# Kernel optimization log

Hardware: AMD Instinct MI355X
Metric: run time of the kernel (lower is better)

Reference implementation:

```python
import jax, jax.numpy as jnp
import numpy as np

N = 50000       # nodes
E = 1600000     # edges
G = 16          # graphs in batch
NUMCHIP = 16    # node features
NUMEDGE = 8     # edge features
H = 32          # hidden_channels
NEG = 0.2       # LeakyReLU slope (PyG GAT default)


def _wegat_conv(x, ea, src, dst, Wn, bn, We, be, att):
    """Edge-weighted GAT conv: returns (node_out [N,H], edge_out [E,NUMEDGE])."""
    xn = x @ Wn + bn                      # [N, H]
    ea2 = ea @ We + be                    # [E, NUMEDGE]
    xi = xn[dst]                          # [E, H] target features
    xj = xn[src]                          # [E, H] source features
    logits = jnp.concatenate([xi, xj, ea2], axis=-1) @ att   # [E]
    logits = jax.nn.leaky_relu(logits, NEG)
    # numerically stable softmax over incoming edges per destination node
    m = jax.ops.segment_max(logits, dst, num_segments=N)
    m = jnp.where(jnp.isfinite(m), m, 0.0)
    p = jnp.exp(logits - m[dst])
    s = jax.ops.segment_sum(p, dst, num_segments=N)
    alpha = p / (s[dst] + 1e-16)          # [E]
    out = jax.ops.segment_sum(xj * alpha[:, None], dst, num_segments=N)  # [N, H]
    return out, ea2


def setup_inputs() -> dict:
    key = jax.random.key(0)
    ks = jax.random.split(key, 24)

    def gl(k, shape):
        fan_in = shape[0] if len(shape) > 1 else shape[0]
        return jax.random.normal(k, shape, dtype=jnp.float32) * (1.0 / np.sqrt(fan_in))

    inp = {
        'x': jax.random.normal(ks[0], (N, NUMCHIP), dtype=jnp.float32),
        'edge_attr': jax.random.normal(ks[1], (E, NUMEDGE), dtype=jnp.float32),
        'edge_index': jax.random.randint(ks[2], (2, E), 0, N, dtype=jnp.int64),
        'batch': jnp.sort(jax.random.randint(ks[3], (N,), 0, G, dtype=jnp.int64)),
        # layer 1
        'Wn1': gl(ks[4], (NUMCHIP, H)), 'bn1': jnp.zeros((H,), jnp.float32),
        'We1': gl(ks[5], (NUMEDGE, NUMEDGE)), 'be1': jnp.zeros((NUMEDGE,), jnp.float32),
        'att1': gl(ks[6], (2 * H + NUMEDGE,)),
        # layer 2
        'Wn2': gl(ks[7], (H, H)), 'bn2': jnp.zeros((H,), jnp.float32),
        'We2': gl(ks[8], (NUMEDGE, NUMEDGE)), 'be2': jnp.zeros((NUMEDGE,), jnp.float32),
        'att2': gl(ks[9], (2 * H + NUMEDGE,)),
        # layer 3
        'Wn3': gl(ks[10], (H, H)), 'bn3': jnp.zeros((H,), jnp.float32),
        'We3': gl(ks[11], (NUMEDGE, NUMEDGE)), 'be3': jnp.zeros((NUMEDGE,), jnp.float32),
        'att3': gl(ks[12], (2 * H + NUMEDGE,)),
        # head
        'Wlin': gl(ks[13], (H, 1)), 'blin': jnp.zeros((1,), jnp.float32),
    }
    return inp


def reference(x, edge_attr, edge_index, batch,
              Wn1, bn1, We1, be1, att1,
              Wn2, bn2, We2, be2, att2,
              Wn3, bn3, We3, be3, att3,
              Wlin, blin):
    src, dst = edge_index[0], edge_index[1]
    x1, ea1 = _wegat_conv(x, edge_attr, src, dst, Wn1, bn1, We1, be1, att1)
    x1 = jax.nn.relu(x1)  # NOTE: original's edge_attr.relu() is a discarded no-op
    x2, ea2 = _wegat_conv(x1, ea1, src, dst, Wn2, bn2, We2, be2, att2)
    x2 = jax.nn.relu(x2)
    x3, _ = _wegat_conv(x2, ea2, src, dst, Wn3, bn3, We3, be3, att3)
    # global mean pool over graphs
    sums = jax.ops.segment_sum(x3, batch, num_segments=G)                   # [G, H]
    cnts = jax.ops.segment_sum(jnp.ones((N,), x3.dtype), batch, num_segments=G)
    pooled = sums / jnp.maximum(cnts, 1.0)[:, None]
    return pooled @ Wlin + blin  # [G, 1]
```

## Files before the change

kernel.cpp:

```cpp
#include <hip/hip_runtime.h>
#include <math.h>


__global__ __launch_bounds__(256) void hist_kernel(const int* __restrict__ dst, int* cnt, int E) {
    int e = blockIdx.x * blockDim.x + threadIdx.x;
    if (e < E) atomicAdd(&cnt[dst[e]], 1);
}

__global__ __launch_bounds__(1024) void scan_kernel(const int* __restrict__ cnt,
                                                    int* rowptr, int* cursor, int n) {
    __shared__ int sums[1024];
    int t = threadIdx.x;
    int CH = (n + 1023) >> 10;
    int s0 = t * CH;
    int s1 = min(n, s0 + CH);
    int local = 0;
    for (int i = s0; i < s1; i++) local += cnt[i];
    sums[t] = local;
    __syncthreads();
    for (int off = 1; off < 1024; off <<= 1) {
        int v = (t >= off) ? sums[t - off] : 0;
        __syncthreads();
        sums[t] += v;
        __syncthreads();
    }
    int run = (t == 0) ? 0 : sums[t - 1];
    for (int i = s0; i < s1; i++) {
        rowptr[i] = run;
        cursor[i] = run;
        run += cnt[i];
    }
    if (t == 1023) rowptr[n] = sums[1023];
}

__global__ __launch_bounds__(256) void scatter_kernel(const int* __restrict__ src,
                                                      const int* __restrict__ dst,
                                                      int* cursor, int2* __restrict__ pack, int E) {
    int e = blockIdx.x * blockDim.x + threadIdx.x;
    if (e >= E) return;
    int d = dst[e];
    int pos = atomicAdd(&cursor[d], 1);
    pack[pos] = make_int2(src[e], e);
}

template <int IN>
__global__ __launch_bounds__(256) void node_linear(const float* __restrict__ xin,
                                                   const float* __restrict__ Wn,
                                                   const float* __restrict__ bn,
                                                   const float* __restrict__ att,
                                                   float* __restrict__ xn,
                                                   float* __restrict__ ai,
                                                   float* __restrict__ aj, int n) {
    int t = blockIdx.x * blockDim.x + threadIdx.x;
    int node = t >> 5;
    int h = t & 31;
    if (node >= n) return;
    float acc = bn[h];
#pragma unroll
    for (int k = 0; k < IN; k++) {
        acc = fmaf(xin[node * IN + k], Wn[k * 32 + h], acc);
    }
    xn[node * 32 + h] = acc;
    float pi = acc * att[h];
    float pj = acc * att[32 + h];
#pragma unroll
    for (int off = 16; off > 0; off >>= 1) {
        pi += __shfl_xor(pi, off);
        pj += __shfl_xor(pj, off);
    }
    if (h == 0) {
        ai[node] = pi;
        aj[node] = pj;
    }
}

__global__ __launch_bounds__(256) void edge_chain(
    const float* __restrict__ ein,
    const float* __restrict__ We1, const float* __restrict__ be1, const float* __restrict__ a1,
    const float* __restrict__ We2, const float* __restrict__ be2, const float* __restrict__ a2,
    const float* __restrict__ We3, const float* __restrict__ be3, const float* __restrict__ a3,
    float* __restrict__ ae1, float* __restrict__ ae2, float* __restrict__ ae3, int E) {
    int e = blockIdx.x * blockDim.x + threadIdx.x;
    if (e >= E) return;
    const float4* p = (const float4*)(ein + (size_t)e * 8);
    float4 x0 = p[0], x1 = p[1];
    float v[8] = {x0.x, x0.y, x0.z, x0.w, x1.x, x1.y, x1.z, x1.w};
    float t[8], u[8];
    float d1 = 0.f, d2 = 0.f, d3 = 0.f;
#pragma unroll
    for (int j = 0; j < 8; j++) {
        float a = be1[j];
#pragma unroll
        for (int k = 0; k < 8; k++) a = fmaf(v[k], We1[k * 8 + j], a);
        t[j] = a;
        d1 = fmaf(a, a1[j], d1);
    }
#pragma unroll
    for (int j = 0; j < 8; j++) {
        float a = be2[j];
#pragma unroll
        for (int k = 0; k < 8; k++) a = fmaf(t[k], We2[k * 8 + j], a);
        u[j] = a;
        d2 = fmaf(a, a2[j], d2);
    }
#pragma unroll
    for (int j = 0; j < 8; j++) {
        float a = be3[j];
#pragma unroll
        for (int k = 0; k < 8; k++) a = fmaf(u[k], We3[k * 8 + j], a);
        d3 = fmaf(a, a3[j], d3);
    }
    ae1[e] = d1;
    ae2[e] = d2;
    ae3[e] = d3;
}

__global__ __launch_bounds__(256) void gat_aggregate(const float* __restrict__ xn,
                                                     const float* __restrict__ ai,
                                                     const float* __restrict__ aj,
                                                     const float* __restrict__ ae,
                                                     const int* __restrict__ rowptr,
                                                     const int2* __restrict__ pack,
                                                     float* __restrict__ xout,
                                                     int n, int relu_out) {
    int wave = (blockIdx.x * blockDim.x + threadIdx.x) >> 6;
    int lane = threadIdx.x & 63;
    if (wave >= n) return;
    int node = wave;
    int row = rowptr[node];
    int deg = rowptr[node + 1] - row;
    int h = lane & 31;
    if (deg == 0) {
        if (lane < 32) xout[node * 32 + h] = 0.f;
        return;
    }
    float a_i = ai[node];
    const int2* pk = pack + row;

    float mx = -INFINITY;
    for (int k = lane; k < deg; k += 64) {
        int2 q = pk[k];
        float lg = a_i + aj[q.x] + ae[q.y];
        lg = (lg >= 0.f) ? lg : 0.2f * lg;
        mx = fmaxf(mx, lg);
    }
#pragma unroll
    for (int off = 32; off > 0; off >>= 1) mx = fmaxf(mx, __shfl_xor(mx, off));

    float acc = 0.f, psum = 0.f;
    int half = lane >> 5;
    for (int base = 0; base < deg; base += 64) {
        int k = base + lane;
        float p = 0.f;
        int s = 0;
        if (k < deg) {
            int2 q = pk[k];
            s = q.x;
            float lg = a_i + aj[s] + ae[q.y];
            lg = (lg >= 0.f) ? lg : 0.2f * lg;
            p = expf(lg - mx);
        }
        psum += p;
        int csize = min(64, deg - base);
        for (int j = half; j < csize; j += 2) {
            float pj = __shfl(p, j);
            int sj = __shfl(s, j);
            acc = fmaf(pj, xn[sj * 32 + h], acc);
        }
    }
#pragma unroll
    for (int off = 32; off > 0; off >>= 1) psum += __shfl_xor(psum, off);
    acc += __shfl_xor(acc, 32);

    float o = acc / (psum + 1e-16f);
    if (relu_out) o = fmaxf(o, 0.f);
    if (lane < 32) xout[node * 32 + h] = o;
}

__global__ __launch_bounds__(256) void pool_kernel(const float* __restrict__ x3,
                                                   const int* __restrict__ batch,
                                                   float* pool, int n) {
    int h = threadIdx.x & 31;
    int rowl = threadIdx.x >> 5;
    int per = (n + gridDim.x - 1) / gridDim.x;
    int n0 = blockIdx.x * per;
    int n1 = min(n, n0 + per);
    float acc = 0.f;
    int curg = -1;
    for (int i = n0 + rowl; i < n1; i += 8) {
        int g = batch[i];
        if (g != curg) {
            if (curg >= 0) atomicAdd(&pool[curg * 32 + h], acc);
            acc = 0.f;
            curg = g;
        }
        acc += x3[i * 32 + h];
    }
    if (curg >= 0) atomicAdd(&pool[curg * 32 + h], acc);
}

__global__ __launch_bounds__(64) void head_kernel(const float* __restrict__ pool,
                                                  const int* __restrict__ batch,
                                                  const float* __restrict__ Wlin,
                                                  const float* __restrict__ blin,
                                                  float* out, int n, int G) {
    int g = threadIdx.x;
    if (g >= G) return;
    float s = 0.f;
#pragma unroll
    for (int k = 0; k < 32; k++) s = fmaf(pool[g * 32 + k], Wlin[k], s);
    int lo = 0, hi = n;
    while (lo < hi) {
        int m = (lo + hi) >> 1;
        if (batch[m] < g) lo = m + 1; else hi = m;
    }
    int start = lo;
    lo = 0; hi = n;
    while (lo < hi) {
        int m = (lo + hi) >> 1;
        if (batch[m] < g + 1) lo = m + 1; else hi = m;
    }
    float c = fmaxf((float)(lo - start), 1.f);
    out[g] = s / c + blin[0];
}

extern "C" void kernel_launch(void* const* d_in, const int* in_sizes, int n_in,
                              void* d_out, int out_size, void* d_ws, size_t ws_size,
                              hipStream_t stream) {
    const float* x    = (const float*)d_in[0];
    const float* ea0  = (const float*)d_in[1];
    const int* ei     = (const int*)d_in[2];
    const int* batch  = (const int*)d_in[3];
    const float* Wn[3] = {(const float*)d_in[4], (const float*)d_in[9],  (const float*)d_in[14]};
    const float* bn[3] = {(const float*)d_in[5], (const float*)d_in[10], (const float*)d_in[15]};
    const float* We[3] = {(const float*)d_in[6], (const float*)d_in[11], (const float*)d_in[16]};
    const float* be[3] = {(const float*)d_in[7], (const float*)d_in[12], (const float*)d_in[17]};
    const float* att[3]= {(const float*)d_in[8], (const float*)d_in[13], (const float*)d_in[18]};
    const float* Wlin = (const float*)d_in[19];
    const float* blin = (const float*)d_in[20];
    float* out = (float*)d_out;

    const int N = in_sizes[0] / 16;
    const int E = in_sizes[1] / 8;
    const int G = out_size;
    (void)n_in; (void)ws_size;

    const int* srcp = ei;
    const int* dstp = ei + E;

    char* base = (char*)d_ws;
    size_t off = 0;
    auto carve = [&](size_t bytes) -> void* {
        void* p = base + off;
        off = (off + bytes + 255) & ~(size_t)255;
        return p;
    };
    float* xnA   = (float*)carve((size_t)N * 32 * 4);
    float* xnB   = (float*)carve((size_t)N * 32 * 4);
    float* ai    = (float*)carve((size_t)N * 4);
    float* aj    = (float*)carve((size_t)N * 4);
    float* ae1   = (float*)carve((size_t)E * 4);
    float* ae2   = (float*)carve((size_t)E * 4);
    float* ae3   = (float*)carve((size_t)E * 4);
    int* cnt     = (int*)carve((size_t)N * 4);
    int* rowptr  = (int*)carve((size_t)(N + 1) * 4);
    int* cursor  = (int*)carve((size_t)N * 4);
    int2* pack   = (int2*)carve((size_t)E * 8);
    float* pool  = (float*)carve((size_t)G * 32 * 4);

    int ebks = (E + 255) / 256;
    int nhbks = (N * 32 + 255) / 256;
    int aggbks = (N + 3) / 4;

    hipMemsetAsync(cnt, 0, (size_t)N * 4, stream);
    hipMemsetAsync(pool, 0, (size_t)G * 32 * 4, stream);
    hist_kernel<<<ebks, 256, 0, stream>>>(dstp, cnt, E);
    scan_kernel<<<1, 1024, 0, stream>>>(cnt, rowptr, cursor, N);
    scatter_kernel<<<ebks, 256, 0, stream>>>(srcp, dstp, cursor, pack, E);

    edge_chain<<<ebks, 256, 0, stream>>>(ea0,
                                         We[0], be[0], att[0] + 64,
                                         We[1], be[1], att[1] + 64,
                                         We[2], be[2], att[2] + 64,
                                         ae1, ae2, ae3, E);

    node_linear<16><<<nhbks, 256, 0, stream>>>(x, Wn[0], bn[0], att[0], xnA, ai, aj, N);
    gat_aggregate<<<aggbks, 256, 0, stream>>>(xnA, ai, aj, ae1, rowptr, pack, xnB, N, 1);

    node_linear<32><<<nhbks, 256, 0, stream>>>(xnB, Wn[1], bn[1], att[1], xnA, ai, aj, N);
    gat_aggregate<<<aggbks, 256, 0, stream>>>(xnA, ai, aj, ae2, rowptr, pack, xnB, N, 1);

    node_linear<32><<<nhbks, 256, 0, stream>>>(xnB, Wn[2], bn[2], att[2], xnA, ai, aj, N);
    gat_aggregate<<<aggbks, 256, 0, stream>>>(xnA, ai, aj, ae3, rowptr, pack, xnB, N, 0);

    pool_kernel<<<128, 256, 0, stream>>>(xnB, batch, pool, N);
    head_kernel<<<1, 64, 0, stream>>>(pool, batch, Wlin, blin, out, N, G);
}
```

Before: 751.1 us.

## Two-level bucket sort of edges with pre-permuted edge logits for aggregation

Replaces the per-destination atomic scatter with a coarse scatter into 32-node buckets followed by a per-bucket shared-memory sort. That sort also gathers the three per-layer edge attention terms into CSR order, so aggregation reads contiguous src and ae arrays instead of doing an indirect ae[e] gather. It also adds a single-pass fast path for nodes with degree at most 64, and aliases the staging buffers with the node feature buffers. Packing dst<<16|src assumes N fits in 16 bits; N=50000 fits, but this is a size-dependent limitation.

```diff
diff --git a/kernel.cpp b/kernel.cpp
--- a/kernel.cpp
+++ b/kernel.cpp
@@ -1,6 +1,8 @@
 #include <hip/hip_runtime.h>
 #include <math.h>
 
+
+#define BSTEP 32
 
 __global__ __launch_bounds__(256) void hist_kernel(const int* __restrict__ dst, int* cnt, int E) {
     int e = blockIdx.x * blockDim.x + threadIdx.x;
@@ -8,7 +10,7 @@
 }
 
 __global__ __launch_bounds__(1024) void scan_kernel(const int* __restrict__ cnt,
-                                                    int* rowptr, int* cursor, int n) {
+                                                    int* rowptr, int n) {
     __shared__ int sums[1024];
     int t = threadIdx.x;
     int CH = (n + 1023) >> 10;
@@ -27,20 +29,57 @@
     int run = (t == 0) ? 0 : sums[t - 1];
     for (int i = s0; i < s1; i++) {
         rowptr[i] = run;
-        cursor[i] = run;
         run += cnt[i];
     }
     if (t == 1023) rowptr[n] = sums[1023];
 }
 
-__global__ __launch_bounds__(256) void scatter_kernel(const int* __restrict__ src,
+__global__ __launch_bounds__(256) void bucket_init(const int* __restrict__ rowptr,
+                                                   int* bcur, int nb, int n) {
+    int b = blockIdx.x * blockDim.x + threadIdx.x;
+    if (b < nb) bcur[b] = rowptr[min(n, b * BSTEP)];
+}
+
+__global__ __launch_bounds__(256) void bucket_scatter(const int* __restrict__ src,
                                                       const int* __restrict__ dst,
-                                                      int* cursor, int2* __restrict__ pack, int E) {
+                                                      int* bcur, int2* __restrict__ stage, int E) {
     int e = blockIdx.x * blockDim.x + threadIdx.x;
     if (e >= E) return;
     int d = dst[e];
-    int pos = atomicAdd(&cursor[d], 1);
-    pack[pos] = make_int2(src[e], e);
+    int pos = atomicAdd(&bcur[d >> 5], 1);
+    stage[pos] = make_int2((int)(((unsigned)d << 16) | (unsigned)src[e]), e);
+}
+
+__global__ __launch_bounds__(256) void bucket_sort(const int2* __restrict__ stage,
+                                                   const int* __restrict__ rowptr,
+                                                   const float* __restrict__ ae1,
+                                                   const float* __restrict__ ae2,
+                                                   const float* __restrict__ ae3,
+                                                   int* __restrict__ srcs,
+                                                   float* __restrict__ aes1,
+                                                   float* __restrict__ aes2,
+                                                   float* __restrict__ aes3, int n) {
+    __shared__ int cur[BSTEP];
+    int b = blockIdx.x;
+    int lo = b * BSTEP;
+    int hi = min(n, lo + BSTEP);
+    int t = threadIdx.x;
+    if (t < hi - lo) cur[t] = rowptr[lo + t];
+    __syncthreads();
+    int s0 = rowptr[lo];
+    int s1 = rowptr[hi];
+    for (int k = s0 + t; k < s1; k += blockDim.x) {
+        int2 q = stage[k];
+        unsigned v = (unsigned)q.x;
+        int d = (int)(v >> 16);
+        int s = (int)(v & 0xFFFFu);
+        int pos = atomicAdd(&cur[d - lo], 1);
+        int e = q.y;
+        srcs[pos] = s;
+        aes1[pos] = ae1[e];
+        aes2[pos] = ae2[e];
+        aes3[pos] = ae3[e];
+    }
 }
 
 template <int IN>
@@ -118,9 +157,9 @@
 __global__ __launch_bounds__(256) void gat_aggregate(const float* __restrict__ xn,
                                                      const float* __restrict__ ai,
                                                      const float* __restrict__ aj,
-                                                     const float* __restrict__ ae,
+                                                     const float* __restrict__ aes,
                                                      const int* __restrict__ rowptr,
-                                                     const int2* __restrict__ pack,
+                                                     const int* __restrict__ srcs,
                                                      float* __restrict__ xout,
                                                      int n, int relu_out) {
     int wave = (blockIdx.x * blockDim.x + threadIdx.x) >> 6;
@@ -135,12 +174,41 @@
         return;
     }
     float a_i = ai[node];
-    const int2* pk = pack + row;
+    const int* sp = srcs + row;
+    const float* ap = aes + row;
+    int half = lane >> 5;
+
+    if (deg <= 64) {
+        int s = 0;
+        float lg = -INFINITY;
+        if (lane < deg) {
+            s = sp[lane];
+            lg = a_i + aj[s] + ap[lane];
+            lg = (lg >= 0.f) ? lg : 0.2f * lg;
+        }
+        float mx = lg;
+#pragma unroll
+        for (int off = 32; off > 0; off >>= 1) mx = fmaxf(mx, __shfl_xor(mx, off));
+        float p = (lane < deg) ? expf(lg - mx) : 0.f;
+        float psum = p;
+#pragma unroll
+        for (int off = 32; off > 0; off >>= 1) psum += __shfl_xor(psum, off);
+        float acc = 0.f;
+        for (int j = half; j < deg; j += 2) {
+            float pj = __shfl(p, j);
+            int sj = __shfl(s, j);
+            acc = fmaf(pj, xn[sj * 32 + h], acc);
+        }
+        acc += __shfl_xor(acc, 32);
+        float o = acc / (psum + 1e-16f);
+        if (relu_out) o = fmaxf(o, 0.f);
+        if (lane < 32) xout[node * 32 + h] = o;
+        return;
+    }
 
     float mx = -INFINITY;
     for (int k = lane; k < deg; k += 64) {
-        int2 q = pk[k];
-        float lg = a_i + aj[q.x] + ae[q.y];
+        float lg = a_i + aj[sp[k]] + ap[k];
         lg = (lg >= 0.f) ? lg : 0.2f * lg;
         mx = fmaxf(mx, lg);
     }
@@ -148,15 +216,13 @@
     for (int off = 32; off > 0; off >>= 1) mx = fmaxf(mx, __shfl_xor(mx, off));
 
     float acc = 0.f, psum = 0.f;
-    int half = lane >> 5;
     for (int base = 0; base < deg; base += 64) {
         int k = base + lane;
         float p = 0.f;
         int s = 0;
         if (k < deg) {
-            int2 q = pk[k];
-            s = q.x;
-            float lg = a_i + aj[s] + ae[q.y];
+            s = sp[k];
+            float lg = a_i + aj[s] + ap[k];
             lg = (lg >= 0.f) ? lg : 0.2f * lg;
             p = expf(lg - mx);
         }
@@ -248,6 +314,8 @@
     const int* srcp = ei;
     const int* dstp = ei + E;
 
+    const int nb = (N + BSTEP - 1) / BSTEP;
+
     char* base = (char*)d_ws;
     size_t off = 0;
     auto carve = [&](size_t bytes) -> void* {
@@ -255,18 +323,24 @@
         off = (off + bytes + 255) & ~(size_t)255;
         return p;
     };
-    float* xnA   = (float*)carve((size_t)N * 32 * 4);
-    float* xnB   = (float*)carve((size_t)N * 32 * 4);
+    float* aes1  = (float*)carve((size_t)E * 4);
+    float* aes2  = (float*)carve((size_t)E * 4);
+    float* aes3  = (float*)carve((size_t)E * 4);
+    int* srcs    = (int*)carve((size_t)E * 4);
     float* ai    = (float*)carve((size_t)N * 4);
     float* aj    = (float*)carve((size_t)N * 4);
-    float* ae1   = (float*)carve((size_t)E * 4);
-    float* ae2   = (float*)carve((size_t)E * 4);
-    float* ae3   = (float*)carve((size_t)E * 4);
     int* cnt     = (int*)carve((size_t)N * 4);
     int* rowptr  = (int*)carve((size_t)(N + 1) * 4);
-    int* cursor  = (int*)carve((size_t)N * 4);
-    int2* pack   = (int2*)carve((size_t)E * 8);
+    int* bcur    = (int*)carve((size_t)nb * 4);
     float* pool  = (float*)carve((size_t)G * 32 * 4);
+
+    char* trans = base + off;
+    int2* stage  = (int2*)trans;
+    float* ae1   = (float*)(trans + (size_t)E * 8);
+    float* ae2   = ae1 + E;
+    float* ae3   = ae2 + E;
+    float* xnA   = (float*)trans;
+    float* xnB   = xnA + (size_t)N * 32;
 
     int ebks = (E + 255) / 256;
     int nhbks = (N * 32 + 255) / 256;
@@ -275,8 +349,9 @@
     hipMemsetAsync(cnt, 0, (size_t)N * 4, stream);
     hipMemsetAsync(pool, 0, (size_t)G * 32 * 4, stream);
     hist_kernel<<<ebks, 256, 0, stream>>>(dstp, cnt, E);
-    scan_kernel<<<1, 1024, 0, stream>>>(cnt, rowptr, cursor, N);
-    scatter_kernel<<<ebks, 256, 0, stream>>>(srcp, dstp, cursor, pack, E);
+    scan_kernel<<<1, 1024, 0, stream>>>(cnt, rowptr, N);
+    bucket_init<<<(nb + 255) / 256, 256, 0, stream>>>(rowptr, bcur, nb, N);
+    bucket_scatter<<<ebks, 256, 0, stream>>>(srcp, dstp, bcur, stage, E);
 
     edge_chain<<<ebks, 256, 0, stream>>>(ea0,
                                          We[0], be[0], att[0] + 64,
@@ -284,14 +359,17 @@
                                          We[2], be[2], att[2] + 64,
                                          ae1, ae2, ae3, E);
 
+    bucket_sort<<<nb, 256, 0, stream>>>(stage, rowptr, ae1, ae2, ae3,
+                                        srcs, aes1, aes2, aes3, N);
+
     node_linear<16><<<nhbks, 256, 0, stream>>>(x, Wn[0], bn[0], att[0], xnA, ai, aj, N);
-    gat_aggregate<<<aggbks, 256, 0, stream>>>(xnA, ai, aj, ae1, rowptr, pack, xnB, N, 1);
+    gat_aggregate<<<aggbks, 256, 0, stream>>>(xnA, ai, aj, aes1, rowptr, srcs, xnB, N, 1);
 
     node_linear<32><<<nhbks, 256, 0, stream>>>(xnB, Wn[1], bn[1], att[1], xnA, ai, aj, N);
-    gat_aggregate<<<aggbks, 256, 0, stream>>>(xnA, ai, aj, ae2, rowptr, pack, xnB, N, 1);
+    gat_aggregate<<<aggbks, 256, 0, stream>>>(xnA, ai, aj, aes2, rowptr, srcs, xnB, N, 1);
 
     node_linear<32><<<nhbks, 256, 0, stream>>>(xnB, Wn[2], bn[2], att[2], xnA, ai, aj, N);
-    gat_aggregate<<<aggbks, 256, 0, stream>>>(xnA, ai, aj, ae3, rowptr, pack, xnB, N, 0);
+    gat_aggregate<<<aggbks, 256, 0, stream>>>(xnA, ai, aj, aes3, rowptr, srcs, xnB, N, 0);
 
     pool_kernel<<<128, 256, 0, stream>>>(xnB, batch, pool, N);
     head_kernel<<<1, 64, 0, stream>>>(pool, batch, Wlin, blin, out, N, G);
```

New measurement: 868.6 us. 1.16x slower.
